# Kernel optimization log

Hardware: AMD Instinct MI355X
Metric: run time of the kernel (lower is better)

## Reference

```python
import jax, jax.numpy as jnp
import numpy as np
from jax import lax

NP = 27  # num_param, perfect cube
N3 = 3   # cube root
EPS = 1e-5


def _conv3d(x, w, stride, pad):
    return lax.conv_general_dilated(
        x, w, window_strides=(stride,) * 3, padding=[(pad, pad)] * 3,
        dimension_numbers=("NCDHW", "OIDHW", "NCDHW"))


def _p_n():
    # torch.meshgrid(arange(3),arange(3),arange(3), indexing='xy') == np.meshgrid 'xy'
    g0, g1, g2 = np.meshgrid(np.arange(N3), np.arange(N3), np.arange(N3), indexing="xy")
    p_n = np.concatenate([g0.ravel(), g1.ravel(), g2.ravel()], 0)  # (3N,)
    return jnp.asarray(p_n, jnp.float32).reshape(1, 3 * NP, 1, 1, 1)


def _p_0(h, w, d):
    # faithful to original: 'xy' meshgrid, flatten, then view(1,1,h,w,d)
    g0, g1, g2 = np.meshgrid(np.arange(h), np.arange(w), np.arange(d), indexing="xy")
    outs = []
    for g in (g0, g1, g2):
        gg = jnp.asarray(g.ravel(), jnp.float32).reshape(1, 1, h, w, d)
        outs.append(jnp.broadcast_to(gg, (1, NP, h, w, d)))
    return jnp.concatenate(outs, axis=1)  # (1, 3N, h, w, d)


def _gather_xq(x_flat, ix, iy, iz, W, D, shape):
    # x_flat: (b, c, H*W*D); i*: (b, h, w, d, N) int32
    idx = ix * (W * D) + iy * D + iz
    b = idx.shape[0]
    idx = jnp.clip(idx, 0, x_flat.shape[-1] - 1).reshape(b, -1)
    xq = jax.vmap(lambda xf, ii: xf[:, ii])(x_flat, idx)  # (b, c, h*w*d*N)
    return xq.reshape(shape)


def reference(x, p_w, p_b, conv_w, gamma, beta):
    b, c, H, W, D = x.shape
    # offset prediction (weight is zero-initialized in original; bias drives offsets)
    offset = _conv3d(x, p_w, 1, 1) + p_b[None, :, None, None, None]  # (b, 3N, h, w, d)
    h, w, d = offset.shape[2:]

    p = _p_0(h, w, d) + _p_n() + offset                 # (b, 3N, h, w, d)
    p = jnp.transpose(p, (0, 2, 3, 4, 1))               # (b, h, w, d, 3N)
    px, py, pz = p[..., :NP], p[..., NP:2 * NP], p[..., 2 * NP:]

    fx, fy, fz = jnp.floor(px), jnp.floor(py), jnp.floor(pz)
    ltx = jnp.clip(fx, 0, H - 1); lty = jnp.clip(fy, 0, W - 1); ltz = jnp.clip(fz, 0, D - 1)
    rbx = jnp.clip(fx + 1, 0, H - 1); rby = jnp.clip(fy + 1, 0, W - 1); rbz = jnp.clip(fz + 1, 0, D - 1)

    pcx = jnp.clip(px, 0, H - 1); pcy = jnp.clip(py, 0, W - 1); pcz = jnp.clip(pz, 0, D - 1)

    # trilinear-style weights (6 corners as in the original)
    g_lt = (1 + (ltx - pcx)) * (1 + (lty - pcy)) * (1 + (ltz - pcz))
    g_rb = (1 - (rbx - pcx)) * (1 - (rby - pcy)) * (1 - (rbz - pcz))
    g_lb = (1 + (ltx - pcx)) * (1 - (rby - pcy)) * (1 + (ltz - pcz))
    g_rt = (1 - (rbx - pcx)) * (1 + (lty - pcy)) * (1 + (ltz - pcz))
    g_lf = (1 + (ltx - pcx)) * (1 + (lty - pcy)) * (1 - (rbz - pcz))
    g_rf = (1 - (rbx - pcx)) * (1 - (rby - pcy)) * (1 + (ltz - pcz))

    i = lambda t: t.astype(jnp.int32)
    x_flat = x.reshape(b, c, -1)
    shp = (b, c, h, w, d, NP)
    xq_lt = _gather_xq(x_flat, i(ltx), i(lty), i(ltz), W, D, shp)
    xq_rb = _gather_xq(x_flat, i(rbx), i(rby), i(rbz), W, D, shp)
    xq_lb = _gather_xq(x_flat, i(ltx), i(rby), i(ltz), W, D, shp)
    xq_rt = _gather_xq(x_flat, i(rbx), i(lty), i(ltz), W, D, shp)
    xq_lf = _gather_xq(x_flat, i(ltx), i(lty), i(rbz), W, D, shp)
    xq_rf = _gather_xq(x_flat, i(rbx), i(rby), i(ltz), W, D, shp)

    e = lambda g: g[:, None]  # (b,1,h,w,d,N)
    x_off = (e(g_lt) * xq_lt + e(g_rb) * xq_rb + e(g_lb) * xq_lb +
             e(g_rt) * xq_rt + e(g_lf) * xq_lf + e(g_rf) * xq_rf)

    # regroup (b,c,h,w,d,27) -> (b,c,3h,3w,3d)
    x_off = x_off.reshape(b, c, h, w, d, N3, N3, N3)
    x_off = jnp.transpose(x_off, (0, 1, 2, 5, 3, 6, 4, 7)).reshape(b, c, h * N3, w * N3, d * N3)

    # Conv3d(stride 2, pad 1, no bias) + BatchNorm3d (train mode, batch stats) + SiLU
    o = _conv3d(x_off, conv_w, 2, 1)
    mean = jnp.mean(o, axis=(0, 2, 3, 4), keepdims=True)
    var = jnp.var(o, axis=(0, 2, 3, 4), keepdims=True)
    y = gamma[None, :, None, None, None] * (o - mean) * lax.rsqrt(var + EPS) + beta[None, :, None, None, None]
    return y * jax.nn.sigmoid(y)


def setup_inputs() -> dict:
    key = jax.random.key(0)
    k1, k2, k3 = jax.random.split(key, 3)
    B, Cin, Cout, S = 2, 16, 32, 32
    x = jax.random.normal(k1, (B, Cin, S, S, S), jnp.float32)
    p_w = jnp.zeros((3 * NP, Cin, 3, 3, 3), jnp.float32)  # zero-init as in original
    bound = 1.0 / np.sqrt(Cin * 27)
    p_b = jax.random.uniform(k2, (3 * NP,), jnp.float32, -bound, bound)
    conv_w = jax.random.normal(k3, (Cout, Cin, 3, 3, 3), jnp.float32) * 0.05
    gamma = jnp.ones((Cout,), jnp.float32)
    beta = jnp.zeros((Cout,), jnp.float32)
    return {"x": x, "p_w": p_w, "p_b": p_b, "conv_w": conv_w, "gamma": gamma, "beta": beta}
```

## Files before the change

### kernel.cpp

```cpp
#include <hip/hip_runtime.h>
#include <hip/hip_bf16.h>

constexpr int BATCH = 2;
constexpr int CIN   = 16;
constexpr int COUT  = 32;
constexpr int HWD   = 32768;
constexpr int BIG   = 96;
constexpr int OUTD  = 48;
constexpr int OUT2  = OUTD * OUTD;
constexpr int OUTN  = OUTD * OUTD * OUTD;
constexpr int NOUT  = BATCH * COUT * OUTN;
constexpr int NBLK3 = 1728;

typedef __attribute__((ext_vector_type(2)))  float f32x2;
typedef __attribute__((ext_vector_type(8)))  short bf16x8;
typedef __attribute__((ext_vector_type(16))) float f32x16;

__device__ __forceinline__ float bf_lo(uint u) { return __uint_as_float(u << 16); }
__device__ __forceinline__ float bf_hi(uint u) { return __uint_as_float(u & 0xFFFF0000u); }
__device__ __forceinline__ f32x2 up2(uint u) {
    f32x2 r; r.x = bf_lo(u); r.y = bf_hi(u); return r;
}

__global__ __launch_bounds__(256) void k_prep(const float* __restrict__ cw,
                                              const float* __restrict__ pw,
                                              const float* __restrict__ x,
                                              ushort* __restrict__ wTb,
                                              ushort* __restrict__ pwTb,
                                              ushort* __restrict__ xb,
                                              uint* __restrict__ lut) {
    int blk = blockIdx.x;
    if (blk < 216) {
        int t = blk * 256 + threadIdx.x;
        if (t < 13824) {
            int ci = t & 15; int rr = t >> 4; int co = rr & 31; int tap = rr >> 5;
            __hip_bfloat16 h = __float2bfloat16(cw[co * 432 + ci * 27 + tap]);
            wTb[t] = *(ushort*)&h;
        } else {
            int u = t - 13824;
            int ci = u & 15; int rr = u >> 4; int oc = rr % 96; int tap = rr / 96;
            float v = (oc < 81) ? pw[oc * 432 + ci * 27 + tap] : 0.f;
            __hip_bfloat16 h = __float2bfloat16(v);
            pwTb[u] = *(ushort*)&h;
        }
    } else if (blk < 222) {
        int s = (blk - 216) * 256 + threadIdx.x;
        if (s < 1445) {
            int su = s / 289; int rm = s - su * 289;
            int sv = rm / 17; int sw = rm - sv * 17;
            lut[s] = (uint)su | ((uint)sv << 8) | ((uint)sw << 16);
        }
    } else {
        int t = (blk - 222) * 256 + threadIdx.x;
        int bt = t >> 15, pos = t & 32767;
        float v[16];
#pragma unroll
        for (int ci = 0; ci < 16; ci++) v[ci] = x[(bt * 16 + ci) * HWD + pos];
        uint uw[8];
#pragma unroll
        for (int cc = 0; cc < 8; cc++) {
            __hip_bfloat16 h0 = __float2bfloat16(v[2 * cc]);
            __hip_bfloat16 h1 = __float2bfloat16(v[2 * cc + 1]);
            uw[cc] = (uint)(*(ushort*)&h0) | ((uint)(*(ushort*)&h1) << 16);
        }
        uint4* xd = (uint4*)(xb + (size_t)t * 16);
        xd[0] = make_uint4(uw[0], uw[1], uw[2], uw[3]);
        xd[1] = make_uint4(uw[4], uw[5], uw[6], uw[7]);
    }
}

__global__ __launch_bounds__(256) void k_offset_mfma(const ushort* __restrict__ xb,
                                                     const ushort* __restrict__ pwTb,
                                                     const float* __restrict__ p_b,
                                                     ushort* __restrict__ offP) {
    __shared__ uint4 repbuf[1728];
    uint4*  lds = repbuf;
    ushort* rep = (ushort*)repbuf;

    int blk = blockIdx.x;
    int bt = blk >> 8; int r = blk & 255;
    int ut = r >> 4; int vt = (r >> 2) & 3; int wt = r & 3;
    int a0 = ut * 2, b0 = vt * 8, c0 = wt * 8;
    int tid = threadIdx.x;
    int wv = tid >> 6, l = tid & 63, col = l & 31, half = l >> 5;

    const ushort* xbb = xb + (size_t)bt * HWD * 16;
    for (int s = tid; s < 800; s += 256) {
        int h = s & 1, p = s >> 1;
        int su = p / 100; int rm = p - su * 100;
        int sv = rm / 10; int sw = rm - sv * 10;
        int ga = a0 - 1 + su, gb = b0 - 1 + sv, gc = c0 - 1 + sw;
        uint4 v = make_uint4(0, 0, 0, 0);
        if ((unsigned)ga < 32u && (unsigned)gb < 32u && (unsigned)gc < 32u)
            v = *(const uint4*)(xbb + (size_t)(ga * 1024 + gb * 32 + gc) * 16 + h * 8);
        lds[((su * 10 + sv) * 11 + sw) * 2 + h] = v;
    }
    __syncthreads();

    int U = wv >> 1, V = ((wv & 1) << 2) + (col >> 3), W = col & 7;
    const uint4* wt4 = (const uint4*)pwTb;

    f32x16 acc[3];
#pragma unroll 1
    for (int g = 0; g < 3; g++) {
        bf16x8 wf[27];
#pragma unroll
        for (int t = 0; t < 27; t++)
            wf[t] = __builtin_bit_cast(bf16x8, wt4[(t * 96 + g * 32 + col) * 2 + half]);
#pragma unroll
        for (int i = 0; i < 16; i++) acc[g][i] = 0.f;
#pragma unroll
        for (int k1 = 0; k1 < 3; k1++)
#pragma unroll
        for (int k2 = 0; k2 < 3; k2++)
#pragma unroll
        for (int k3 = 0; k3 < 3; k3++) {
            bf16x8 xf = __builtin_bit_cast(bf16x8,
                lds[(((U + k1) * 10 + (V + k2)) * 11 + (W + k3)) * 2 + half]);
            acc[g] = __builtin_amdgcn_mfma_f32_32x32x16_bf16(wf[(k1 * 3 + k2) * 3 + k3],
                                                             xf, acc[g], 0, 0, 0);
        }
    }
    __syncthreads();

    int posl = (U * 8 + V) * 8 + W;
#pragma unroll 1
    for (int g = 0; g < 3; g++) {
#pragma unroll
        for (int rg = 0; rg < 16; rg++) {
            int co = g * 32 + (rg & 3) + 8 * (rg >> 2) + 4 * half;
            if (co < 81) {
                int n = co % 27, d = co / 27;
                __hip_bfloat16 h = __float2bfloat16(acc[g][rg] + p_b[co]);
                rep[posl * 108 + n * 4 + d] = *(ushort*)&h;
            }
        }
    }
    __syncthreads();

    const uint* rp = (const uint*)rep;
    uint* og = (uint*)offP + (size_t)bt * HWD * 54;
    for (int f = tid; f < 6912; f += 256) {
        int pl = f / 54; int i = f - pl * 54;
        int pu = pl >> 6, pv = (pl >> 3) & 7, pw2 = pl & 7;
        int pos = (a0 + pu) * 1024 + (b0 + pv) * 32 + (c0 + pw2);
        og[(size_t)pos * 54 + i] = rp[f];
    }
}

__global__ __launch_bounds__(256, 2) void k_fused(const ushort* __restrict__ xb,
                                                  const ushort* __restrict__ offP,
                                                  const ushort* __restrict__ wTb,
                                                  const uint* __restrict__ lut,
                                                  ushort* __restrict__ o16,
                                                  float* __restrict__ psum,
                                                  float* __restrict__ psq) {
    __shared__ uint4 halo[5 * 17 * 19 * 2];
    __shared__ uint4 xbox[847 * 2];
    __shared__ float ls[4][32], lq[4][32];

    int blk = (blockIdx.x & 7) * 216 + (blockIdx.x >> 3);

    int bt = blk / 864; int r = blk - bt * 864;
    int ut = r / 36; r -= ut * 36;
    int vt = r / 6;  int wt = r - vt * 6;

    int tid = threadIdx.x;
    int wv = tid >> 6, l = tid & 63;
    int col = l & 31, half = l >> 5;

    int gU0 = ut * 4 - 1, gV0 = vt * 16 - 1, gW0 = wt * 16 - 1;
    int bx0 = (gV0 < 0 ? 0 : gV0 / 3) - 1;
    int ay0 = (gU0 < 0 ? 0 : gU0 / 3) - 1;
    int cz0 = (gW0 < 0 ? 0 : gW0 / 3) - 1;

    const ushort* xbb = xb + (size_t)bt * HWD * 16;

    for (int s = tid; s < 847; s += 256) {
        int dx = s / 77; int rm = s - dx * 77;
        int dy = rm / 11; int dz = rm - dy * 11;
        int X = bx0 + dx; X = X < 0 ? 0 : (X > 31 ? 31 : X);
        int Y = ay0 + dy; Y = Y < 0 ? 0 : (Y > 31 ? 31 : Y);
        int Z = cz0 + dz; Z = Z < 0 ? 0 : (Z > 31 ? 31 : Z);
        const uint4* src = (const uint4*)(xbb + (size_t)(X * 1024 + Y * 32 + Z) * 16);
        xbox[s * 2]     = src[0];
        xbox[s * 2 + 1] = src[1];
    }
    __syncthreads();

    const ushort* offb = offP + (size_t)bt * HWD * 108;
    for (int s = tid; s < 1445; s += 256) {
        uint code = lut[s];
        int su = code & 255, sv = (code >> 8) & 255, sw = code >> 16;
        int gU = gU0 + su, gV = gV0 + sv, gW = gW0 + sw;
        uint4 r0 = make_uint4(0, 0, 0, 0), r1 = r0;
        if (gU >= 0 && gV >= 0 && gW >= 0) {
            int a = gU / 3, i = gU - a * 3;
            int b = gV / 3, j = gV - b * 3;
            int c = gW / 3, kk = gW - c * 3;
            int n = i * 9 + j * 3 + kk;
            int pos = a * 1024 + b * 32 + c;
            uint2 ou = *(const uint2*)(offb + (size_t)pos * 108 + n * 4);
            float ox = bf_lo(ou.x), oy = bf_hi(ou.x), oz = bf_lo(ou.y);

            float px = (float)(b + j) + ox;
            float py = (float)(a + i) + oy;
            float pz = (float)(c + kk) + oz;

            float fx = floorf(px), fy = floorf(py), fz = floorf(pz);
            float ltx = fminf(fmaxf(fx, 0.f), 31.f);
            float lty = fminf(fmaxf(fy, 0.f), 31.f);
            float ltz = fminf(fmaxf(fz, 0.f), 31.f);
            float rbx = fminf(fmaxf(fx + 1.f, 0.f), 31.f);
            float rby = fminf(fmaxf(fy + 1.f, 0.f), 31.f);
            float rbz = fminf(fmaxf(fz + 1.f, 0.f), 31.f);
            float pcx = fminf(fmaxf(px, 0.f), 31.f);
            float pcy = fminf(fmaxf(py, 0.f), 31.f);
            float pcz = fminf(fmaxf(pz, 0.f), 31.f);

            float axl = 1.f + (ltx - pcx), axr = 1.f - (rbx - pcx);
            float ayl = 1.f + (lty - pcy), ayr = 1.f - (rby - pcy);
            float azl = 1.f + (ltz - pcz), azr = 1.f - (rbz - pcz);

            float g_lt = axl * ayl * azl;
            float g_rb = axr * ayr * azr;
            float g_lb = axl * ayr * azl;
            float g_rt = axr * ayl * azl;
            float g_lf = axl * ayl * azr;
            float g_rf = axr * ayr * azl;

            int sxl = (int)ltx - bx0, sxr = (int)rbx - bx0;
            int syl = (int)lty - ay0, syr = (int)rby - ay0;
            int szl = (int)ltz - cz0, szr = (int)rbz - cz0;

            int c_lt = (sxl * 7 + syl) * 11 + szl;
            int c_rb = (sxr * 7 + syr) * 11 + szr;
            int c_lb = (sxl * 7 + syr) * 11 + szl;
            int c_rt = (sxr * 7 + syl) * 11 + szl;
            int c_lf = (sxl * 7 + syl) * 11 + szr;
            int c_rf = (sxr * 7 + syr) * 11 + szl;

            f32x2 acc2[8];
#pragma unroll
            for (int q = 0; q < 8; q++) acc2[q] = (f32x2){0.f, 0.f};

            auto corner = [&](float g, int ci2) {
                uint4 u0 = xbox[ci2 * 2], u1 = xbox[ci2 * 2 + 1];
                f32x2 g2 = {g, g};
                acc2[0] += g2 * up2(u0.x); acc2[1] += g2 * up2(u0.y);
                acc2[2] += g2 * up2(u0.z); acc2[3] += g2 * up2(u0.w);
                acc2[4] += g2 * up2(u1.x); acc2[5] += g2 * up2(u1.y);
                acc2[6] += g2 * up2(u1.z); acc2[7] += g2 * up2(u1.w);
            };
            corner(g_lt, c_lt);
            corner(g_rb, c_rb);
            corner(g_lb, c_lb);
            corner(g_rt, c_rt);
            corner(g_lf, c_lf);
            corner(g_rf, c_rf);

            uint uw[8];
#pragma unroll
            for (int cc = 0; cc < 8; cc++) {
                __hip_bfloat16 h0 = __float2bfloat16(acc2[cc].x);
                __hip_bfloat16 h1 = __float2bfloat16(acc2[cc].y);
                uw[cc] = (uint)(*(ushort*)&h0) | ((uint)(*(ushort*)&h1) << 16);
            }
            r0 = make_uint4(uw[0], uw[1], uw[2], uw[3]);
            r1 = make_uint4(uw[4], uw[5], uw[6], uw[7]);
        }
        int slot = (sw & 1) * 9 + (sw >> 1);
        halo[((su * 17 + sv) * 19 + slot) * 2 + 0] = r0;
        halo[((su * 17 + sv) * 19 + slot) * 2 + 1] = r1;
    }

    bf16x8 wf[27];
    const uint4* wt4 = (const uint4*)wTb;
#pragma unroll
    for (int t = 0; t < 27; t++)
        wf[t] = __builtin_bit_cast(bf16x8, wt4[(t * 32 + col) * 2 + half]);

    __syncthreads();

    int U = wv >> 1, V = (wv & 1) * 4 + (col >> 3), W = col & 7;
    const uint4* lp = &halo[(((2 * U * 17 + 2 * V) * 19) + W) * 2 + half];

    f32x16 acc;
#pragma unroll
    for (int i = 0; i < 16; i++) acc[i] = 0.f;

#pragma unroll
    for (int k1 = 0; k1 < 3; k1++)
#pragma unroll
    for (int k2 = 0; k2 < 3; k2++)
#pragma unroll
    for (int k3 = 0; k3 < 3; k3++) {
        const int so = (k3 == 0) ? 0 : (k3 == 1 ? 9 : 1);
        const int off2 = ((k1 * 17 + k2) * 19 + so) * 2;
        bf16x8 xf = __builtin_bit_cast(bf16x8, lp[off2]);
        acc = __builtin_amdgcn_mfma_f32_32x32x16_bf16(wf[(k1 * 3 + k2) * 3 + k3],
                                                      xf, acc, 0, 0, 0);
    }

    int u = ut * 2 + U, v = vt * 8 + V, wg = wt * 8 + W;
    size_t posg = (size_t)u * OUT2 + v * OUTD + wg;
    ushort* ob = o16 + (size_t)bt * COUT * OUTN;
#pragma unroll
    for (int rg = 0; rg < 16; rg++) {
        int co = (rg & 3) + 8 * (rg >> 2) + 4 * half;
        __hip_bfloat16 h = __float2bfloat16(acc[rg]);
        ob[(size_t)co * OUTN + posg] = *(ushort*)&h;
    }

#pragma unroll
    for (int rg = 0; rg < 16; rg++) {
        float s = acc[rg], q = acc[rg] * acc[rg];
#pragma unroll
        for (int o = 1; o < 32; o <<= 1) {
            s += __shfl_xor(s, o);
            q += __shfl_xor(q, o);
        }
        if (col == 0) {
            int co = (rg & 3) + 8 * (rg >> 2) + 4 * half;
            ls[wv][co] = s; lq[wv][co] = q;
        }
    }
    __syncthreads();
    if (tid < 32) {
        float s = ls[0][tid] + ls[1][tid] + ls[2][tid] + ls[3][tid];
        float q = lq[0][tid] + lq[1][tid] + lq[2][tid] + lq[3][tid];
        psum[blk * 32 + tid] = s;
        psq[blk * 32 + tid]  = q;
    }
}

__global__ __launch_bounds__(256) void k_stats(const float* __restrict__ psum,
                                               const float* __restrict__ psq,
                                               const float* __restrict__ gamma,
                                               const float* __restrict__ beta,
                                               float* __restrict__ stats) {
    int co  = blockIdx.x;
    int tid = threadIdx.x;
    float s = 0.f, q = 0.f;
    for (int i = tid; i < NBLK3; i += 256) {
        s += psum[i * 32 + co];
        q += psq[i * 32 + co];
    }
    __shared__ float ss[256], sq[256];
    ss[tid] = s; sq[tid] = q;
    __syncthreads();
    for (int st = 128; st > 0; st >>= 1) {
        if (tid < st) { ss[tid] += ss[tid + st]; sq[tid] += sq[tid + st]; }
        __syncthreads();
    }
    if (tid == 0) {
        const float N = 221184.f;
        float mean = ss[0] / N;
        float var  = sq[0] / N - mean * mean;
        float inv  = rsqrtf(var + 1e-5f);
        float A = gamma[co] * inv;
        stats[co * 2]     = A;
        stats[co * 2 + 1] = beta[co] - A * mean;
    }
}

__global__ __launch_bounds__(256) void k_bn_silu(const ushort* __restrict__ o16,
                                                 const float* __restrict__ stats,
                                                 float* __restrict__ out) {
    int t = blockIdx.x * 256 + threadIdx.x;
    int co = (t / (OUTN / 8)) & 31;
    float A = stats[co * 2], B = stats[co * 2 + 1];
    uint4 u = ((const uint4*)o16)[t];
    float o[8] = {bf_lo(u.x), bf_hi(u.x), bf_lo(u.y), bf_hi(u.y),
                  bf_lo(u.z), bf_hi(u.z), bf_lo(u.w), bf_hi(u.w)};
    float y[8];
#pragma unroll
    for (int q = 0; q < 8; q++) {
        float yy = A * o[q] + B;
        y[q] = yy / (1.f + __expf(-yy));
    }
    float4* dst = (float4*)(out + (size_t)t * 8);
    dst[0] = make_float4(y[0], y[1], y[2], y[3]);
    dst[1] = make_float4(y[4], y[5], y[6], y[7]);
}

extern "C" void kernel_launch(void* const* d_in, const int* in_sizes, int n_in,
                              void* d_out, int out_size, void* d_ws, size_t ws_size,
                              hipStream_t stream) {
    const float* x      = (const float*)d_in[0];
    const float* p_w    = (const float*)d_in[1];
    const float* p_b    = (const float*)d_in[2];
    const float* conv_w = (const float*)d_in[3];
    const float* gamma  = (const float*)d_in[4];
    const float* beta   = (const float*)d_in[5];
    float* out = (float*)d_out;
    float* ws  = (float*)d_ws;

    float* psum  = ws;
    float* psq   = psum + 55296;
    float* stats = psq + 55296;
    ushort* wTb  = (ushort*)(stats + 64);
    ushort* pwTb = wTb + 13824;
    ushort* xb   = pwTb + 41472;
    ushort* offP = xb + 1048576;
    ushort* o16  = offP + 7077888;
    uint*   lut  = (uint*)(o16 + 7077888);

    k_prep<<<478, 256, 0, stream>>>(conv_w, p_w, x, wTb, pwTb, xb, lut);
    k_offset_mfma<<<512, 256, 0, stream>>>(xb, pwTb, p_b, offP);
    k_fused<<<NBLK3, 256, 0, stream>>>(xb, offP, wTb, lut, o16, psum, psq);
    k_stats<<<32, 256, 0, stream>>>(psum, psq, gamma, beta, stats);
    k_bn_silu<<<NOUT / 2048, 256, 0, stream>>>(o16, stats, out);
}
```

Measured before the change: 111.2 us.

## Drop shared xbox staging; gather deformable corners directly from global memory

Removes the shared-memory staging of an 847-voxel input box and its block barrier, and reads the six bilinear corners for each sample directly from global bf16 input, relying on L1/L2 caching. The halo-slot permutation moves into the precomputed LUT, the boundary branch becomes a multiplicative validity mask so every thread runs straight-line code, and launch bounds ask for 3 blocks per SIMD since LDS use drops. The trade is more global and L2 traffic and latency on the gather in return for higher occupancy and one fewer sync.

```diff
diff --git a/kernel.cpp b/kernel.cpp
--- a/kernel.cpp
+++ b/kernel.cpp
@@ -44,11 +44,12 @@
             pwTb[u] = *(ushort*)&h;
         }
     } else if (blk < 222) {
-        int s = (blk - 216) * 256 + threadIdx.x;
-        if (s < 1445) {
-            int su = s / 289; int rm = s - su * 289;
-            int sv = rm / 17; int sw = rm - sv * 17;
-            lut[s] = (uint)su | ((uint)sv << 8) | ((uint)sw << 16);
+        int e = (blk - 216) * 256 + threadIdx.x;
+        if (e < 1445) {
+            int su = e / 289; int rm = e - su * 289;
+            int sv = rm / 17; int ts = rm - sv * 17;
+            int sw = (ts < 9) ? (2 * ts) : (2 * ts - 17);
+            lut[e] = (uint)su | ((uint)sv << 8) | ((uint)sw << 16) | ((uint)ts << 24);
         }
     } else {
         int t = (blk - 222) * 256 + threadIdx.x;
@@ -148,7 +149,7 @@
     }
 }
 
-__global__ __launch_bounds__(256, 2) void k_fused(const ushort* __restrict__ xb,
+__global__ __launch_bounds__(256, 3) void k_fused(const ushort* __restrict__ xb,
                                                   const ushort* __restrict__ offP,
                                                   const ushort* __restrict__ wTb,
                                                   const uint* __restrict__ lut,
@@ -156,7 +157,6 @@
                                                   float* __restrict__ psum,
                                                   float* __restrict__ psq) {
     __shared__ uint4 halo[5 * 17 * 19 * 2];
-    __shared__ uint4 xbox[847 * 2];
     __shared__ float ls[4][32], lq[4][32];
 
     int blk = (blockIdx.x & 7) * 216 + (blockIdx.x >> 3);
@@ -170,108 +170,91 @@
     int col = l & 31, half = l >> 5;
 
     int gU0 = ut * 4 - 1, gV0 = vt * 16 - 1, gW0 = wt * 16 - 1;
-    int bx0 = (gV0 < 0 ? 0 : gV0 / 3) - 1;
-    int ay0 = (gU0 < 0 ? 0 : gU0 / 3) - 1;
-    int cz0 = (gW0 < 0 ? 0 : gW0 / 3) - 1;
-
-    const ushort* xbb = xb + (size_t)bt * HWD * 16;
-
-    for (int s = tid; s < 847; s += 256) {
-        int dx = s / 77; int rm = s - dx * 77;
-        int dy = rm / 11; int dz = rm - dy * 11;
-        int X = bx0 + dx; X = X < 0 ? 0 : (X > 31 ? 31 : X);
-        int Y = ay0 + dy; Y = Y < 0 ? 0 : (Y > 31 ? 31 : Y);
-        int Z = cz0 + dz; Z = Z < 0 ? 0 : (Z > 31 ? 31 : Z);
-        const uint4* src = (const uint4*)(xbb + (size_t)(X * 1024 + Y * 32 + Z) * 16);
-        xbox[s * 2]     = src[0];
-        xbox[s * 2 + 1] = src[1];
-    }
-    __syncthreads();
-
+    const ushort* xbb  = xb + (size_t)bt * HWD * 16;
     const ushort* offb = offP + (size_t)bt * HWD * 108;
+
     for (int s = tid; s < 1445; s += 256) {
         uint code = lut[s];
-        int su = code & 255, sv = (code >> 8) & 255, sw = code >> 16;
+        int su = code & 255, sv = (code >> 8) & 255;
+        int sw = (code >> 16) & 255, ts = code >> 24;
         int gU = gU0 + su, gV = gV0 + sv, gW = gW0 + sw;
-        uint4 r0 = make_uint4(0, 0, 0, 0), r1 = r0;
-        if (gU >= 0 && gV >= 0 && gW >= 0) {
-            int a = gU / 3, i = gU - a * 3;
-            int b = gV / 3, j = gV - b * 3;
-            int c = gW / 3, kk = gW - c * 3;
-            int n = i * 9 + j * 3 + kk;
-            int pos = a * 1024 + b * 32 + c;
-            uint2 ou = *(const uint2*)(offb + (size_t)pos * 108 + n * 4);
-            float ox = bf_lo(ou.x), oy = bf_hi(ou.x), oz = bf_lo(ou.y);
-
-            float px = (float)(b + j) + ox;
-            float py = (float)(a + i) + oy;
-            float pz = (float)(c + kk) + oz;
-
-            float fx = floorf(px), fy = floorf(py), fz = floorf(pz);
-            float ltx = fminf(fmaxf(fx, 0.f), 31.f);
-            float lty = fminf(fmaxf(fy, 0.f), 31.f);
-            float ltz = fminf(fmaxf(fz, 0.f), 31.f);
-            float rbx = fminf(fmaxf(fx + 1.f, 0.f), 31.f);
-            float rby = fminf(fmaxf(fy + 1.f, 0.f), 31.f);
-            float rbz = fminf(fmaxf(fz + 1.f, 0.f), 31.f);
-            float pcx = fminf(fmaxf(px, 0.f), 31.f);
-            float pcy = fminf(fmaxf(py, 0.f), 31.f);
-            float pcz = fminf(fmaxf(pz, 0.f), 31.f);
-
-            float axl = 1.f + (ltx - pcx), axr = 1.f - (rbx - pcx);
-            float ayl = 1.f + (lty - pcy), ayr = 1.f - (rby - pcy);
-            float azl = 1.f + (ltz - pcz), azr = 1.f - (rbz - pcz);
-
-            float g_lt = axl * ayl * azl;
-            float g_rb = axr * ayr * azr;
-            float g_lb = axl * ayr * azl;
-            float g_rt = axr * ayl * azl;
-            float g_lf = axl * ayl * azr;
-            float g_rf = axr * ayr * azl;
-
-            int sxl = (int)ltx - bx0, sxr = (int)rbx - bx0;
-            int syl = (int)lty - ay0, syr = (int)rby - ay0;
-            int szl = (int)ltz - cz0, szr = (int)rbz - cz0;
-
-            int c_lt = (sxl * 7 + syl) * 11 + szl;
-            int c_rb = (sxr * 7 + syr) * 11 + szr;
-            int c_lb = (sxl * 7 + syr) * 11 + szl;
-            int c_rt = (sxr * 7 + syl) * 11 + szl;
-            int c_lf = (sxl * 7 + syl) * 11 + szr;
-            int c_rf = (sxr * 7 + syr) * 11 + szl;
-
-            f32x2 acc2[8];
-#pragma unroll
-            for (int q = 0; q < 8; q++) acc2[q] = (f32x2){0.f, 0.f};
-
-            auto corner = [&](float g, int ci2) {
-                uint4 u0 = xbox[ci2 * 2], u1 = xbox[ci2 * 2 + 1];
-                f32x2 g2 = {g, g};
-                acc2[0] += g2 * up2(u0.x); acc2[1] += g2 * up2(u0.y);
-                acc2[2] += g2 * up2(u0.z); acc2[3] += g2 * up2(u0.w);
-                acc2[4] += g2 * up2(u1.x); acc2[5] += g2 * up2(u1.y);
-                acc2[6] += g2 * up2(u1.z); acc2[7] += g2 * up2(u1.w);
-            };
-            corner(g_lt, c_lt);
-            corner(g_rb, c_rb);
-            corner(g_lb, c_lb);
-            corner(g_rt, c_rt);
-            corner(g_lf, c_lf);
-            corner(g_rf, c_rf);
-
-            uint uw[8];
-#pragma unroll
-            for (int cc = 0; cc < 8; cc++) {
-                __hip_bfloat16 h0 = __float2bfloat16(acc2[cc].x);
-                __hip_bfloat16 h1 = __float2bfloat16(acc2[cc].y);
-                uw[cc] = (uint)(*(ushort*)&h0) | ((uint)(*(ushort*)&h1) << 16);
-            }
-            r0 = make_uint4(uw[0], uw[1], uw[2], uw[3]);
-            r1 = make_uint4(uw[4], uw[5], uw[6], uw[7]);
-        }
-        int slot = (sw & 1) * 9 + (sw >> 1);
-        halo[((su * 17 + sv) * 19 + slot) * 2 + 0] = r0;
-        halo[((su * 17 + sv) * 19 + slot) * 2 + 1] = r1;
+        float vf = ((gU | gV | gW) >= 0) ? 1.f : 0.f;
+        unsigned uU = (unsigned)max(gU, 0);
+        unsigned uV = (unsigned)max(gV, 0);
+        unsigned uW = (unsigned)max(gW, 0);
+        int a = uU / 3u, i = uU - 3u * a;
+        int b = uV / 3u, j = uV - 3u * b;
+        int c = uW / 3u, kk = uW - 3u * c;
+        int n = i * 9 + j * 3 + kk;
+        int pos = a * 1024 + b * 32 + c;
+        uint2 ou = *(const uint2*)(offb + (size_t)pos * 108 + n * 4);
+        float ox = bf_lo(ou.x), oy = bf_hi(ou.x), oz = bf_lo(ou.y);
+
+        float px = (float)(b + j) + ox;
+        float py = (float)(a + i) + oy;
+        float pz = (float)(c + kk) + oz;
+
+        float fx = floorf(px), fy = floorf(py), fz = floorf(pz);
+        float ltx = fminf(fmaxf(fx, 0.f), 31.f);
+        float lty = fminf(fmaxf(fy, 0.f), 31.f);
+        float ltz = fminf(fmaxf(fz, 0.f), 31.f);
+        float rbx = fminf(fmaxf(fx + 1.f, 0.f), 31.f);
+        float rby = fminf(fmaxf(fy + 1.f, 0.f), 31.f);
+        float rbz = fminf(fmaxf(fz + 1.f, 0.f), 31.f);
+        float pcx = fminf(fmaxf(px, 0.f), 31.f);
+        float pcy = fminf(fmaxf(py, 0.f), 31.f);
+        float pcz = fminf(fmaxf(pz, 0.f), 31.f);
+
+        float axl = (1.f + (ltx - pcx)) * vf, axr = (1.f - (rbx - pcx)) * vf;
+        float ayl = 1.f + (lty - pcy), ayr = 1.f - (rby - pcy);
+        float azl = 1.f + (ltz - pcz), azr = 1.f - (rbz - pcz);
+
+        float g_lt = axl * ayl * azl;
+        float g_rb = axr * ayr * azr;
+        float g_lb = axl * ayr * azl;
+        float g_rt = axr * ayl * azl;
+        float g_lf = axl * ayl * azr;
+        float g_rf = axr * ayr * azl;
+
+        int iltx = (int)ltx, ilty = (int)lty, iltz = (int)ltz;
+        int irbx = (int)rbx, irby = (int)rby, irbz = (int)rbz;
+
+        int i_lt = iltx * 1024 + ilty * 32 + iltz;
+        int i_rb = irbx * 1024 + irby * 32 + irbz;
+        int i_lb = iltx * 1024 + irby * 32 + iltz;
+        int i_rt = irbx * 1024 + ilty * 32 + iltz;
+        int i_lf = iltx * 1024 + ilty * 32 + irbz;
+        int i_rf = irbx * 1024 + irby * 32 + iltz;
+
+        f32x2 acc2[8];
+#pragma unroll
+        for (int q = 0; q < 8; q++) acc2[q] = (f32x2){0.f, 0.f};
+
+        auto corner = [&](float g, int ip) {
+            const uint4* p = (const uint4*)(xbb + (size_t)ip * 16);
+            uint4 u0 = p[0], u1 = p[1];
+            f32x2 g2 = {g, g};
+            acc2[0] += g2 * up2(u0.x); acc2[1] += g2 * up2(u0.y);
+            acc2[2] += g2 * up2(u0.z); acc2[3] += g2 * up2(u0.w);
+            acc2[4] += g2 * up2(u1.x); acc2[5] += g2 * up2(u1.y);
+            acc2[6] += g2 * up2(u1.z); acc2[7] += g2 * up2(u1.w);
+        };
+        corner(g_lt, i_lt);
+        corner(g_rb, i_rb);
+        corner(g_lb, i_lb);
+        corner(g_rt, i_rt);
+        corner(g_lf, i_lf);
+        corner(g_rf, i_rf);
+
+        uint uw[8];
+#pragma unroll
+        for (int cc = 0; cc < 8; cc++) {
+            __hip_bfloat16 h0 = __float2bfloat16(acc2[cc].x);
+            __hip_bfloat16 h1 = __float2bfloat16(acc2[cc].y);
+            uw[cc] = (uint)(*(ushort*)&h0) | ((uint)(*(ushort*)&h1) << 16);
+        }
+        halo[((su * 17 + sv) * 19 + ts) * 2 + 0] = make_uint4(uw[0], uw[1], uw[2], uw[3]);
+        halo[((su * 17 + sv) * 19 + ts) * 2 + 1] = make_uint4(uw[4], uw[5], uw[6], uw[7]);
     }
 
     bf16x8 wf[27];
```

Measured after the change: 107.0 us. 3.8% less time.
